# Optimization experiments

Measured on AMD Instinct MI355X. Metric: run time of the kernel, lower is better.

Reference implementation:

```python
import jax, jax.numpy as jnp
import numpy as np

N_HEADS = 16
D_K = 64
D_V = 64
HIDDEN = 1024
B, S = 2, 2048
LN_EPS = 1e-5


def setup_inputs() -> dict:
    key = jax.random.key(0)
    ks = jax.random.split(key, 6)
    inputs = jax.random.normal(ks[0], (B, S, HIDDEN), dtype=jnp.float32)
    attn_mask = jax.random.randint(ks[1], (B, S, S), 0, 2, dtype=jnp.int32)
    scale = 1.0 / np.sqrt(HIDDEN)
    W_Q = jax.random.normal(ks[2], (HIDDEN, HIDDEN), dtype=jnp.float32) * scale
    W_K = jax.random.normal(ks[3], (HIDDEN, HIDDEN), dtype=jnp.float32) * scale
    W_V = jax.random.normal(ks[4], (HIDDEN, HIDDEN), dtype=jnp.float32) * scale
    W_O = jax.random.normal(ks[5], (HIDDEN, HIDDEN), dtype=jnp.float32) * scale
    return {"inputs": inputs, "attn_mask": attn_mask,
            "W_Q": W_Q, "W_K": W_K, "W_V": W_V, "W_O": W_O}


def reference(inputs, attn_mask, W_Q, W_K, W_V, W_O):
    b, s, _ = inputs.shape
    # nn.Linear(bias=False): x @ W.T ; reshape to [B, H, S, d]
    Q = (inputs @ W_Q.T).reshape(b, s, N_HEADS, D_K).transpose(0, 2, 1, 3)
    K = (inputs @ W_K.T).reshape(b, s, N_HEADS, D_K).transpose(0, 2, 1, 3)
    V = (inputs @ W_V.T).reshape(b, s, N_HEADS, D_V).transpose(0, 2, 1, 3)
    scores = jnp.einsum('bhqd,bhkd->bhqk', Q, K) / np.sqrt(D_K)
    mask = (attn_mask == 0)[:, None, :, :]  # broadcast over heads
    scores = jnp.where(mask, jnp.float32(-1e9), scores)
    attn = jax.nn.softmax(scores, axis=-1)
    context = jnp.einsum('bhqk,bhkd->bhqd', attn, V)
    context = context.transpose(0, 2, 1, 3).reshape(b, s, N_HEADS * D_V)
    output = context @ W_O.T
    x = output + inputs  # residual
    # LayerNorm with default weight=1, bias=0, eps=1e-5
    mu = jnp.mean(x, axis=-1, keepdims=True)
    var = jnp.mean(jnp.square(x - mu), axis=-1, keepdims=True)
    out = (x - mu) * jax.lax.rsqrt(var + LN_EPS)
    return out, attn
```

## Files before the change

### kernel.cpp

```cpp
#include <hip/hip_runtime.h>

typedef unsigned short u16;
typedef unsigned long long u64;
typedef __bf16 bf16x8 __attribute__((ext_vector_type(8)));
typedef float f32x4 __attribute__((ext_vector_type(4)));

static __device__ __forceinline__ u16 f32_to_bf16(float f) {
    unsigned u = __builtin_bit_cast(unsigned, f);
    u += 0x7fffu + ((u >> 16) & 1u);
    return (u16)(u >> 16);
}
static __device__ __forceinline__ float bf16_to_f32(u16 v) {
    return __builtin_bit_cast(float, ((unsigned)v) << 16);
}

__global__ __launch_bounds__(256) void cast_f32_bf16(const float* __restrict__ in,
                                                     u16* __restrict__ out, int n)
{
    int i = (blockIdx.x * 256 + threadIdx.x) * 4;
    if (i >= n) return;
    float4 v = *reinterpret_cast<const float4*>(in + i);
    ushort4 o;
    o.x = f32_to_bf16(v.x); o.y = f32_to_bf16(v.y);
    o.z = f32_to_bf16(v.z); o.w = f32_to_bf16(v.w);
    *reinterpret_cast<ushort4*>(out + i) = o;
}

__global__ __launch_bounds__(256) void cast_w4(
    const float* __restrict__ w0, const float* __restrict__ w1,
    const float* __restrict__ w2, const float* __restrict__ w3,
    u16* __restrict__ o0, u16* __restrict__ o1,
    u16* __restrict__ o2, u16* __restrict__ o3)
{
    const float* src; u16* dst;
    switch (blockIdx.y) {
        case 0: src = w0; dst = o0; break;
        case 1: src = w1; dst = o1; break;
        case 2: src = w2; dst = o2; break;
        default: src = w3; dst = o3; break;
    }
    int i = (blockIdx.x * 256 + threadIdx.x) * 4;
    float4 v = *reinterpret_cast<const float4*>(src + i);
    ushort4 o;
    o.x = f32_to_bf16(v.x); o.y = f32_to_bf16(v.y);
    o.z = f32_to_bf16(v.z); o.w = f32_to_bf16(v.w);
    *reinterpret_cast<ushort4*>(dst + i) = o;
}

__global__ __launch_bounds__(256) void pack_mask(const int* __restrict__ mask,
                                                 u64* __restrict__ out)
{
    int t = blockIdx.x * 256 + threadIdx.x;
    const int4* p = reinterpret_cast<const int4*>(mask + (size_t)t * 64);
    u64 bits = 0;
#pragma unroll
    for (int j = 0; j < 16; ++j) {
        int4 v = p[j];
        bits |= ((u64)(v.x != 0)) << (j * 4 + 0);
        bits |= ((u64)(v.y != 0)) << (j * 4 + 1);
        bits |= ((u64)(v.z != 0)) << (j * 4 + 2);
        bits |= ((u64)(v.w != 0)) << (j * 4 + 3);
    }
    out[t] = bits;
}

__global__ __launch_bounds__(256) void gemm128_qkv(
    const u16* __restrict__ A,
    const u16* __restrict__ BQ, const u16* __restrict__ BK, const u16* __restrict__ BV,
    u16* __restrict__ CQ, u16* __restrict__ CK, u16* __restrict__ CV)
{
    constexpr int N = 1024, K = 1024;
    const u16* B; u16* C;
    switch (blockIdx.z) {
        case 0:  B = BQ; C = CQ; break;
        case 1:  B = BK; C = CK; break;
        default: B = BV; C = CV; break;
    }
    __shared__ __align__(16) u16 As[128][64];
    __shared__ __align__(16) u16 Bs[128][64];
    const int tid  = threadIdx.x;
    const int wave = tid >> 6, lane = tid & 63;
    const int quad = lane >> 4, l16 = lane & 15;
    const int wr = wave >> 1, wc = wave & 1;
    const int m0 = blockIdx.y * 128, n0 = blockIdx.x * 128;

    f32x4 acc[4][4] = {};
    const int srow = tid >> 3;
    const int scol = (tid & 7) * 8;
    const u16* Ap = A + (size_t)(m0 + srow) * K + scol;
    const u16* Bp = B + (size_t)(n0 + srow) * K + scol;
    u16* AsW = &As[0][0] + wave * 512;
    u16* BsW = &Bs[0][0] + wave * 512;

    for (int k0 = 0; k0 < K; k0 += 64) {
        __syncthreads();
#pragma unroll
        for (int j = 0; j < 4; ++j) {
            __builtin_amdgcn_global_load_lds(
                (const __attribute__((address_space(1))) unsigned*)(Ap + (size_t)(32 * j) * K + k0),
                (__attribute__((address_space(3))) unsigned*)(AsW + j * 2048),
                16, 0, 0);
            __builtin_amdgcn_global_load_lds(
                (const __attribute__((address_space(1))) unsigned*)(Bp + (size_t)(32 * j) * K + k0),
                (__attribute__((address_space(3))) unsigned*)(BsW + j * 2048),
                16, 0, 0);
        }
        __syncthreads();
#pragma unroll
        for (int ks = 0; ks < 2; ++ks) {
            bf16x8 a[4], bb[4];
#pragma unroll
            for (int mi = 0; mi < 4; ++mi)
                a[mi] = *reinterpret_cast<const bf16x8*>(&As[wr * 64 + mi * 16 + l16][ks * 32 + quad * 8]);
#pragma unroll
            for (int ni = 0; ni < 4; ++ni)
                bb[ni] = *reinterpret_cast<const bf16x8*>(&Bs[wc * 64 + ni * 16 + l16][ks * 32 + quad * 8]);
#pragma unroll
            for (int mi = 0; mi < 4; ++mi)
#pragma unroll
                for (int ni = 0; ni < 4; ++ni)
                    acc[mi][ni] = __builtin_amdgcn_mfma_f32_16x16x32_bf16(a[mi], bb[ni], acc[mi][ni], 0, 0, 0);
        }
    }
#pragma unroll
    for (int mi = 0; mi < 4; ++mi)
#pragma unroll
        for (int ni = 0; ni < 4; ++ni)
#pragma unroll
            for (int r = 0; r < 4; ++r) {
                int row = m0 + wr * 64 + mi * 16 + quad * 4 + r;
                int col = n0 + wc * 64 + ni * 16 + l16;
                C[(size_t)row * N + col] = f32_to_bf16(acc[mi][ni][r]);
            }
}

__global__ __launch_bounds__(256) void gemm128_res(
    const u16* __restrict__ A, const u16* __restrict__ B,
    const float* __restrict__ X, float* __restrict__ C)
{
    constexpr int N = 1024, K = 1024;
    __shared__ __align__(16) u16 As[128][64];
    __shared__ __align__(16) u16 Bs[128][64];
    const int tid  = threadIdx.x;
    const int wave = tid >> 6, lane = tid & 63;
    const int quad = lane >> 4, l16 = lane & 15;
    const int wr = wave >> 1, wc = wave & 1;
    const int m0 = blockIdx.y * 128, n0 = blockIdx.x * 128;

    f32x4 acc[4][4] = {};
    const int srow = tid >> 3;
    const int scol = (tid & 7) * 8;
    const u16* Ap = A + (size_t)(m0 + srow) * K + scol;
    const u16* Bp = B + (size_t)(n0 + srow) * K + scol;
    u16* AsW = &As[0][0] + wave * 512;
    u16* BsW = &Bs[0][0] + wave * 512;

    for (int k0 = 0; k0 < K; k0 += 64) {
        __syncthreads();
#pragma unroll
        for (int j = 0; j < 4; ++j) {
            __builtin_amdgcn_global_load_lds(
                (const __attribute__((address_space(1))) unsigned*)(Ap + (size_t)(32 * j) * K + k0),
                (__attribute__((address_space(3))) unsigned*)(AsW + j * 2048),
                16, 0, 0);
            __builtin_amdgcn_global_load_lds(
                (const __attribute__((address_space(1))) unsigned*)(Bp + (size_t)(32 * j) * K + k0),
                (__attribute__((address_space(3))) unsigned*)(BsW + j * 2048),
                16, 0, 0);
        }
        __syncthreads();
#pragma unroll
        for (int ks = 0; ks < 2; ++ks) {
            bf16x8 a[4], bb[4];
#pragma unroll
            for (int mi = 0; mi < 4; ++mi)
                a[mi] = *reinterpret_cast<const bf16x8*>(&As[wr * 64 + mi * 16 + l16][ks * 32 + quad * 8]);
#pragma unroll
            for (int ni = 0; ni < 4; ++ni)
                bb[ni] = *reinterpret_cast<const bf16x8*>(&Bs[wc * 64 + ni * 16 + l16][ks * 32 + quad * 8]);
#pragma unroll
            for (int mi = 0; mi < 4; ++mi)
#pragma unroll
                for (int ni = 0; ni < 4; ++ni)
                    acc[mi][ni] = __builtin_amdgcn_mfma_f32_16x16x32_bf16(a[mi], bb[ni], acc[mi][ni], 0, 0, 0);
        }
    }
#pragma unroll
    for (int mi = 0; mi < 4; ++mi)
#pragma unroll
        for (int ni = 0; ni < 4; ++ni)
#pragma unroll
            for (int r = 0; r < 4; ++r) {
                int row = m0 + wr * 64 + mi * 16 + quad * 4 + r;
                int col = n0 + wc * 64 + ni * 16 + l16;
                C[(size_t)row * N + col] = acc[mi][ni][r] + X[(size_t)row * N + col];
            }
}

__global__ __launch_bounds__(256) void transpose_v(const u16* __restrict__ Vw,
                                                   u16* __restrict__ VT)
{
    constexpr int S = 2048, HID = 1024, NH = 16;
    __shared__ __align__(16) u16 Ts[64][72];
    const int tid = threadIdx.x;
    const int lr = tid >> 2, lc = (tid & 3) * 16;
    const int st = blockIdx.x, h = blockIdx.y, b = blockIdx.z;
    {
        const u16* p = Vw + ((size_t)(b * S + st * 64 + lr)) * HID + h * 64 + lc;
        *reinterpret_cast<int4*>(&Ts[lr][lc])     = *reinterpret_cast<const int4*>(p);
        *reinterpret_cast<int4*>(&Ts[lr][lc + 8]) = *reinterpret_cast<const int4*>(p + 8);
    }
    __syncthreads();
    u16* q = VT + ((size_t)((b * NH + h) * 64 + lr)) * S + st * 64 + lc;
    union { int4 v; u16 s[8]; } o0, o1;
#pragma unroll
    for (int j = 0; j < 8; ++j) o0.s[j] = Ts[lc + j][lr];
#pragma unroll
    for (int j = 0; j < 8; ++j) o1.s[j] = Ts[lc + 8 + j][lr];
    *reinterpret_cast<int4*>(q)     = o0.v;
    *reinterpret_cast<int4*>(q + 8) = o1.v;
}

__global__ __launch_bounds__(256) void attn_kernel(
    const u16* __restrict__ Q, const u16* __restrict__ K,
    const u16* __restrict__ VT, const u64* __restrict__ Mb,
    float* __restrict__ attn_out, u16* __restrict__ ctx_out)
{
    constexpr int S = 2048, HID = 1024, NH = 16;
    __shared__ __align__(16) u16 Qs[64][72];
    __shared__ __align__(16) u16 Ks[64][72];
    __shared__ __align__(16) u16 Vs[64][72];
    __shared__ __align__(16) u16 Ps[64][72];

    const int tid  = threadIdx.x;
    const int wave = tid >> 6, lane = tid & 63;
    const int quad = lane >> 4, l16 = lane & 15;

    const int flat = (blockIdx.z * NH + blockIdx.y) * (S / 64) + blockIdx.x;
    const int s_id = (flat & 7) * 128 + (flat >> 3);
    const int qt = s_id & 31, h = (s_id >> 5) & 15, b = s_id >> 9;

    const size_t qkv_base = (size_t)b * S * HID + h * 64;
    const size_t vt_base  = ((size_t)(b * NH + h)) * 64 * S;

    const int lr = tid >> 2;
    const int lc = (tid & 3) * 16;
    {
        const u16* p = Q + qkv_base + (size_t)(qt * 64 + lr) * HID + lc;
        *reinterpret_cast<int4*>(&Qs[lr][lc])     = *reinterpret_cast<const int4*>(p);
        *reinterpret_cast<int4*>(&Qs[lr][lc + 8]) = *reinterpret_cast<const int4*>(p + 8);
    }

    const int q_row0 = qt * 64 + wave * 16 + quad * 4;
    const size_t mrow = (size_t)b * S + q_row0;

    const u16* Kp = K + qkv_base + (size_t)lr * HID + lc;
    const u16* Vp = VT + vt_base + (size_t)lr * S + lc;

    float l_acc[4] = {0.f, 0.f, 0.f, 0.f};

    int4 kc0 = *reinterpret_cast<const int4*>(Kp);
    int4 kc1 = *reinterpret_cast<const int4*>(Kp + 8);
    for (int kt = 0; kt < S / 64; ++kt) {
        u64 mw[4];
#pragma unroll
        for (int r = 0; r < 4; ++r) mw[r] = Mb[(mrow + r) * 32 + kt];
        __syncthreads();
        *reinterpret_cast<int4*>(&Ks[lr][lc])     = kc0;
        *reinterpret_cast<int4*>(&Ks[lr][lc + 8]) = kc1;
        int4 kn0, kn1;
        if (kt < S / 64 - 1) {
            const u16* p = Kp + (size_t)(kt + 1) * 64 * HID;
            kn0 = *reinterpret_cast<const int4*>(p);
            kn1 = *reinterpret_cast<const int4*>(p + 8);
        } else { kn0 = kc0; kn1 = kc1; }
        __syncthreads();
        f32x4 sc[4] = {};
#pragma unroll
        for (int ks = 0; ks < 2; ++ks) {
            bf16x8 a = *reinterpret_cast<const bf16x8*>(&Qs[wave * 16 + l16][ks * 32 + quad * 8]);
#pragma unroll
            for (int cb = 0; cb < 4; ++cb) {
                bf16x8 bb = *reinterpret_cast<const bf16x8*>(&Ks[cb * 16 + l16][ks * 32 + quad * 8]);
                sc[cb] = __builtin_amdgcn_mfma_f32_16x16x32_bf16(a, bb, sc[cb], 0, 0, 0);
            }
        }
#pragma unroll
        for (int cb = 0; cb < 4; ++cb) {
            int bi = cb * 16 + l16;
#pragma unroll
            for (int r = 0; r < 4; ++r) {
                float pe = ((mw[r] >> bi) & 1ull)
                               ? __expf(fmaf(sc[cb][r], 0.125f, -16.f)) : 0.f;
                l_acc[r] += pe;
            }
        }
        kc0 = kn0; kc1 = kn1;
    }
    float rl[4];
#pragma unroll
    for (int r = 0; r < 4; ++r) {
        float s = l_acc[r];
        s += __shfl_xor(s, 1);
        s += __shfl_xor(s, 2);
        s += __shfl_xor(s, 4);
        s += __shfl_xor(s, 8);
        rl[r] = 1.0f / s;
    }

    f32x4 ctx[4] = {};
    kc0 = *reinterpret_cast<const int4*>(Kp);
    kc1 = *reinterpret_cast<const int4*>(Kp + 8);
    int4 vc0 = *reinterpret_cast<const int4*>(Vp);
    int4 vc1 = *reinterpret_cast<const int4*>(Vp + 8);
    for (int kt = 0; kt < S / 64; ++kt) {
        u64 mw[4];
#pragma unroll
        for (int r = 0; r < 4; ++r) mw[r] = Mb[(mrow + r) * 32 + kt];
        __syncthreads();
        *reinterpret_cast<int4*>(&Ks[lr][lc])     = kc0;
        *reinterpret_cast<int4*>(&Ks[lr][lc + 8]) = kc1;
        *reinterpret_cast<int4*>(&Vs[lr][lc])     = vc0;
        *reinterpret_cast<int4*>(&Vs[lr][lc + 8]) = vc1;
        int4 kn0, kn1, vn0, vn1;
        if (kt < S / 64 - 1) {
            const u16* p = Kp + (size_t)(kt + 1) * 64 * HID;
            kn0 = *reinterpret_cast<const int4*>(p);
            kn1 = *reinterpret_cast<const int4*>(p + 8);
            const u16* pv = Vp + (kt + 1) * 64;
            vn0 = *reinterpret_cast<const int4*>(pv);
            vn1 = *reinterpret_cast<const int4*>(pv + 8);
        } else { kn0 = kc0; kn1 = kc1; vn0 = vc0; vn1 = vc1; }
        __syncthreads();
        f32x4 sc[4] = {};
#pragma unroll
        for (int ks = 0; ks < 2; ++ks) {
            bf16x8 a = *reinterpret_cast<const bf16x8*>(&Qs[wave * 16 + l16][ks * 32 + quad * 8]);
#pragma unroll
            for (int cb = 0; cb < 4; ++cb) {
                bf16x8 bb = *reinterpret_cast<const bf16x8*>(&Ks[cb * 16 + l16][ks * 32 + quad * 8]);
                sc[cb] = __builtin_amdgcn_mfma_f32_16x16x32_bf16(a, bb, sc[cb], 0, 0, 0);
            }
        }
#pragma unroll
        for (int cb = 0; cb < 4; ++cb) {
            int bi = cb * 16 + l16;
#pragma unroll
            for (int r = 0; r < 4; ++r) {
                float pe = ((mw[r] >> bi) & 1ull)
                               ? __expf(fmaf(sc[cb][r], 0.125f, -16.f)) * rl[r] : 0.f;
                Ps[wave * 16 + quad * 4 + r][cb * 16 + l16] = f32_to_bf16(pe);
            }
        }
        asm volatile("s_waitcnt lgkmcnt(0)" ::: "memory");
        __builtin_amdgcn_sched_barrier(0);
        {
            size_t arow = (((size_t)(b * NH + h) * S) + qt * 64 + lr) * S + kt * 64 + lc;
#pragma unroll
            for (int g = 0; g < 4; ++g) {
                float4 o;
                o.x = bf16_to_f32(Ps[lr][lc + g * 4 + 0]);
                o.y = bf16_to_f32(Ps[lr][lc + g * 4 + 1]);
                o.z = bf16_to_f32(Ps[lr][lc + g * 4 + 2]);
                o.w = bf16_to_f32(Ps[lr][lc + g * 4 + 3]);
                *reinterpret_cast<float4*>(&attn_out[arow + g * 4]) = o;
            }
        }
#pragma unroll
        for (int ks = 0; ks < 2; ++ks) {
            bf16x8 a = *reinterpret_cast<const bf16x8*>(&Ps[wave * 16 + l16][ks * 32 + quad * 8]);
#pragma unroll
            for (int cb = 0; cb < 4; ++cb) {
                bf16x8 bb = *reinterpret_cast<const bf16x8*>(&Vs[cb * 16 + l16][ks * 32 + quad * 8]);
                ctx[cb] = __builtin_amdgcn_mfma_f32_16x16x32_bf16(a, bb, ctx[cb], 0, 0, 0);
            }
        }
        kc0 = kn0; kc1 = kn1; vc0 = vn0; vc1 = vn1;
    }
#pragma unroll
    for (int cb = 0; cb < 4; ++cb)
#pragma unroll
        for (int r = 0; r < 4; ++r) {
            int q = q_row0 + r;
            int d = cb * 16 + l16;
            ctx_out[qkv_base + (size_t)q * HID + d] = f32_to_bf16(ctx[cb][r]);
        }
}

__global__ __launch_bounds__(256) void ln_kernel(const float* __restrict__ X,
                                                 float* __restrict__ out)
{
    __shared__ float red[8];
    const int row = blockIdx.x;
    const int tid = threadIdx.x;
    const int wave = tid >> 6, lane = tid & 63;
    const float* xr = X + (size_t)row * 1024;
    float v[4];
    float s = 0.f;
#pragma unroll
    for (int i = 0; i < 4; ++i) { v[i] = xr[tid + 256 * i]; s += v[i]; }
#pragma unroll
    for (int off = 1; off < 64; off <<= 1) s += __shfl_xor(s, off);
    if (lane == 0) red[wave] = s;
    __syncthreads();
    float mean = (red[0] + red[1] + red[2] + red[3]) * (1.0f / 1024.0f);
    float s2 = 0.f;
#pragma unroll
    for (int i = 0; i < 4; ++i) { float d = v[i] - mean; s2 += d * d; }
#pragma unroll
    for (int off = 1; off < 64; off <<= 1) s2 += __shfl_xor(s2, off);
    if (lane == 0) red[4 + wave] = s2;
    __syncthreads();
    float var = (red[4] + red[5] + red[6] + red[7]) * (1.0f / 1024.0f);
    float rstd = rsqrtf(var + 1e-5f);
#pragma unroll
    for (int i = 0; i < 4; ++i)
        out[(size_t)row * 1024 + tid + 256 * i] = (v[i] - mean) * rstd;
}

extern "C" void kernel_launch(void* const* d_in, const int* in_sizes, int n_in,
                              void* d_out, int out_size, void* d_ws, size_t ws_size,
                              hipStream_t stream)
{
    constexpr int B = 2, S = 2048, HID = 1024, NH = 16;
    constexpr int M = B * S;

    const float* X  = (const float*)d_in[0];
    const int* mask = (const int*)d_in[1];
    const float* WQ = (const float*)d_in[2];
    const float* WK = (const float*)d_in[3];
    const float* WV = (const float*)d_in[4];
    const float* WO = (const float*)d_in[5];

    float* out  = (float*)d_out;
    float* attn = out + (size_t)M * HID;

    u64*   Mb  = (u64*)d_ws;
    u16*   Xb  = (u16*)(Mb + (size_t)B * S * 32);
    u16*   WQb = Xb  + (size_t)M * HID;
    u16*   WKb = WQb + (size_t)HID * HID;
    u16*   WVb = WKb + (size_t)HID * HID;
    u16*   WOb = WVb + (size_t)HID * HID;
    u16*   Qw  = WOb + (size_t)HID * HID;
    u16*   Kw  = Qw  + (size_t)M * HID;
    u16*   Vw  = Kw  + (size_t)M * HID;
    u16*   Cw  = Vw  + (size_t)M * HID;
    u16*   VT  = Xb;
    float* XO  = (float*)Qw;

    dim3 blk(256);
    cast_f32_bf16<<<dim3((M * HID) / 1024), blk, 0, stream>>>(X, Xb, M * HID);
    cast_w4<<<dim3((HID * HID) / 1024, 4), blk, 0, stream>>>(WQ, WK, WV, WO,
                                                             WQb, WKb, WVb, WOb);
    pack_mask<<<dim3((B * S * 32) / 256), blk, 0, stream>>>(mask, Mb);

    gemm128_qkv<<<dim3(HID / 128, M / 128, 3), blk, 0, stream>>>(Xb, WQb, WKb, WVb,
                                                                 Qw, Kw, Vw);
    transpose_v<<<dim3(S / 64, NH, B), blk, 0, stream>>>(Vw, VT);

    attn_kernel<<<dim3(S / 64, NH, B), blk, 0, stream>>>(Qw, Kw, VT, Mb, attn, Cw);

    gemm128_res<<<dim3(HID / 128, M / 128), blk, 0, stream>>>(Cw, WOb, X, XO);
    ln_kernel<<<dim3(M), blk, 0, stream>>>(XO, out);
}
```

Before: 844.7 us.

## Pre-swizzle K and V into MFMA fragment layout, load directly to registers

A prep kernel now rewrites K and V into per-tile MFMA operand order, replacing the old V transpose. The attention kernel then loads K and V fragments straight from global memory into registers and keeps Q fragments in registers. This removes the shared-memory staging and two barriers per tile. The trade-off is that each of the four waves now fetches the full K/V tile separately and the explicit software prefetch is gone, so latency hiding depends on cache hits and occupancy. The extra Vf buffer also enlarges the workspace.

Measured after the change: 880.9 us. 4.3% more time.

```diff
diff --git a/kernel.cpp b/kernel.cpp
--- a/kernel.cpp
+++ b/kernel.cpp
@@ -197,39 +197,47 @@
             }
 }
 
-__global__ __launch_bounds__(256) void transpose_v(const u16* __restrict__ Vw,
-                                                   u16* __restrict__ VT)
+__global__ __launch_bounds__(256) void prep_kv(const u16* __restrict__ Kw,
+                                               const u16* __restrict__ Vw,
+                                               u16* __restrict__ Kf,
+                                               u16* __restrict__ Vf)
 {
     constexpr int S = 2048, HID = 1024, NH = 16;
-    __shared__ __align__(16) u16 Ts[64][72];
+    __shared__ __align__(16) u16 Kt[64][72];
+    __shared__ __align__(16) u16 Vt[64][72];
     const int tid = threadIdx.x;
+    const int kt = blockIdx.x, h = blockIdx.y, b = blockIdx.z;
     const int lr = tid >> 2, lc = (tid & 3) * 16;
-    const int st = blockIdx.x, h = blockIdx.y, b = blockIdx.z;
     {
-        const u16* p = Vw + ((size_t)(b * S + st * 64 + lr)) * HID + h * 64 + lc;
-        *reinterpret_cast<int4*>(&Ts[lr][lc])     = *reinterpret_cast<const int4*>(p);
-        *reinterpret_cast<int4*>(&Ts[lr][lc + 8]) = *reinterpret_cast<const int4*>(p + 8);
+        const u16* pk = Kw + ((size_t)(b * S + kt * 64 + lr)) * HID + h * 64 + lc;
+        *reinterpret_cast<int4*>(&Kt[lr][lc])     = *reinterpret_cast<const int4*>(pk);
+        *reinterpret_cast<int4*>(&Kt[lr][lc + 8]) = *reinterpret_cast<const int4*>(pk + 8);
+        const u16* pv = Vw + ((size_t)(b * S + kt * 64 + lr)) * HID + h * 64 + lc;
+        *reinterpret_cast<int4*>(&Vt[lr][lc])     = *reinterpret_cast<const int4*>(pv);
+        *reinterpret_cast<int4*>(&Vt[lr][lc + 8]) = *reinterpret_cast<const int4*>(pv + 8);
     }
     __syncthreads();
-    u16* q = VT + ((size_t)((b * NH + h) * 64 + lr)) * S + st * 64 + lc;
-    union { int4 v; u16 s[8]; } o0, o1;
-#pragma unroll
-    for (int j = 0; j < 8; ++j) o0.s[j] = Ts[lc + j][lr];
-#pragma unroll
-    for (int j = 0; j < 8; ++j) o1.s[j] = Ts[lc + 8 + j][lr];
-    *reinterpret_cast<int4*>(q)     = o0.v;
-    *reinterpret_cast<int4*>(q + 8) = o1.v;
+    const size_t fbase = (((size_t)(b * NH + h)) * 32 + kt) * 4096;
+    for (int c = tid; c < 512; c += 256) {
+        int frag = c >> 6;
+        int lane = c & 63;
+        int l16 = lane & 15, quad = lane >> 4;
+        int ks = frag >> 2, cb = frag & 3;
+        *reinterpret_cast<int4*>(Kf + fbase + (size_t)c * 8) =
+            *reinterpret_cast<const int4*>(&Kt[cb * 16 + l16][ks * 32 + quad * 8]);
+        u16 tmp[8];
+#pragma unroll
+        for (int e = 0; e < 8; ++e) tmp[e] = Vt[ks * 32 + quad * 8 + e][cb * 16 + l16];
+        *reinterpret_cast<int4*>(Vf + fbase + (size_t)c * 8) = *reinterpret_cast<int4*>(tmp);
+    }
 }
 
 __global__ __launch_bounds__(256) void attn_kernel(
-    const u16* __restrict__ Q, const u16* __restrict__ K,
-    const u16* __restrict__ VT, const u64* __restrict__ Mb,
+    const u16* __restrict__ Qw, const u16* __restrict__ Kf,
+    const u16* __restrict__ Vf, const u64* __restrict__ Mb,
     float* __restrict__ attn_out, u16* __restrict__ ctx_out)
 {
     constexpr int S = 2048, HID = 1024, NH = 16;
-    __shared__ __align__(16) u16 Qs[64][72];
-    __shared__ __align__(16) u16 Ks[64][72];
-    __shared__ __align__(16) u16 Vs[64][72];
     __shared__ __align__(16) u16 Ps[64][72];
 
     const int tid  = threadIdx.x;
@@ -241,50 +249,34 @@
     const int qt = s_id & 31, h = (s_id >> 5) & 15, b = s_id >> 9;
 
     const size_t qkv_base = (size_t)b * S * HID + h * 64;
-    const size_t vt_base  = ((size_t)(b * NH + h)) * 64 * S;
-
-    const int lr = tid >> 2;
-    const int lc = (tid & 3) * 16;
-    {
-        const u16* p = Q + qkv_base + (size_t)(qt * 64 + lr) * HID + lc;
-        *reinterpret_cast<int4*>(&Qs[lr][lc])     = *reinterpret_cast<const int4*>(p);
-        *reinterpret_cast<int4*>(&Qs[lr][lc + 8]) = *reinterpret_cast<const int4*>(p + 8);
-    }
+    const size_t f_base   = ((size_t)(b * NH + h)) * 131072;
+
+    bf16x8 qf[2];
+#pragma unroll
+    for (int ks = 0; ks < 2; ++ks)
+        qf[ks] = *reinterpret_cast<const bf16x8*>(
+            Qw + qkv_base + (size_t)(qt * 64 + wave * 16 + l16) * HID + ks * 32 + quad * 8);
 
     const int q_row0 = qt * 64 + wave * 16 + quad * 4;
     const size_t mrow = (size_t)b * S + q_row0;
 
-    const u16* Kp = K + qkv_base + (size_t)lr * HID + lc;
-    const u16* Vp = VT + vt_base + (size_t)lr * S + lc;
-
     float l_acc[4] = {0.f, 0.f, 0.f, 0.f};
 
-    int4 kc0 = *reinterpret_cast<const int4*>(Kp);
-    int4 kc1 = *reinterpret_cast<const int4*>(Kp + 8);
     for (int kt = 0; kt < S / 64; ++kt) {
+        const u16* kfp = Kf + f_base + (size_t)kt * 4096 + lane * 8;
+        bf16x8 kf[8];
+#pragma unroll
+        for (int f = 0; f < 8; ++f)
+            kf[f] = *reinterpret_cast<const bf16x8*>(kfp + f * 512);
         u64 mw[4];
 #pragma unroll
         for (int r = 0; r < 4; ++r) mw[r] = Mb[(mrow + r) * 32 + kt];
-        __syncthreads();
-        *reinterpret_cast<int4*>(&Ks[lr][lc])     = kc0;
-        *reinterpret_cast<int4*>(&Ks[lr][lc + 8]) = kc1;
-        int4 kn0, kn1;
-        if (kt < S / 64 - 1) {
-            const u16* p = Kp + (size_t)(kt + 1) * 64 * HID;
-            kn0 = *reinterpret_cast<const int4*>(p);
-            kn1 = *reinterpret_cast<const int4*>(p + 8);
-        } else { kn0 = kc0; kn1 = kc1; }
-        __syncthreads();
         f32x4 sc[4] = {};
 #pragma unroll
-        for (int ks = 0; ks < 2; ++ks) {
-            bf16x8 a = *reinterpret_cast<const bf16x8*>(&Qs[wave * 16 + l16][ks * 32 + quad * 8]);
-#pragma unroll
-            for (int cb = 0; cb < 4; ++cb) {
-                bf16x8 bb = *reinterpret_cast<const bf16x8*>(&Ks[cb * 16 + l16][ks * 32 + quad * 8]);
-                sc[cb] = __builtin_amdgcn_mfma_f32_16x16x32_bf16(a, bb, sc[cb], 0, 0, 0);
-            }
-        }
+        for (int ks = 0; ks < 2; ++ks)
+#pragma unroll
+            for (int cb = 0; cb < 4; ++cb)
+                sc[cb] = __builtin_amdgcn_mfma_f32_16x16x32_bf16(qf[ks], kf[ks * 4 + cb], sc[cb], 0, 0, 0);
 #pragma unroll
         for (int cb = 0; cb < 4; ++cb) {
             int bi = cb * 16 + l16;
@@ -295,7 +287,6 @@
                 l_acc[r] += pe;
             }
         }
-        kc0 = kn0; kc1 = kn1;
     }
     float rl[4];
 #pragma unroll
@@ -308,40 +299,27 @@
         rl[r] = 1.0f / s;
     }
 
+    const int lr = tid >> 2;
+    const int lc = (tid & 3) * 16;
     f32x4 ctx[4] = {};
-    kc0 = *reinterpret_cast<const int4*>(Kp);
-    kc1 = *reinterpret_cast<const int4*>(Kp + 8);
-    int4 vc0 = *reinterpret_cast<const int4*>(Vp);
-    int4 vc1 = *reinterpret_cast<const int4*>(Vp + 8);
     for (int kt = 0; kt < S / 64; ++kt) {
+        const u16* kfp = Kf + f_base + (size_t)kt * 4096 + lane * 8;
+        const u16* vfp = Vf + f_base + (size_t)kt * 4096 + lane * 8;
+        bf16x8 kf[8], vf[8];
+#pragma unroll
+        for (int f = 0; f < 8; ++f) {
+            kf[f] = *reinterpret_cast<const bf16x8*>(kfp + f * 512);
+            vf[f] = *reinterpret_cast<const bf16x8*>(vfp + f * 512);
+        }
         u64 mw[4];
 #pragma unroll
         for (int r = 0; r < 4; ++r) mw[r] = Mb[(mrow + r) * 32 + kt];
-        __syncthreads();
-        *reinterpret_cast<int4*>(&Ks[lr][lc])     = kc0;
-        *reinterpret_cast<int4*>(&Ks[lr][lc + 8]) = kc1;
-        *reinterpret_cast<int4*>(&Vs[lr][lc])     = vc0;
-        *reinterpret_cast<int4*>(&Vs[lr][lc + 8]) = vc1;
-        int4 kn0, kn1, vn0, vn1;
-        if (kt < S / 64 - 1) {
-            const u16* p = Kp + (size_t)(kt + 1) * 64 * HID;
-            kn0 = *reinterpret_cast<const int4*>(p);
-            kn1 = *reinterpret_cast<const int4*>(p + 8);
-            const u16* pv = Vp + (kt + 1) * 64;
-            vn0 = *reinterpret_cast<const int4*>(pv);
-            vn1 = *reinterpret_cast<const int4*>(pv + 8);
-        } else { kn0 = kc0; kn1 = kc1; vn0 = vc0; vn1 = vc1; }
-        __syncthreads();
         f32x4 sc[4] = {};
 #pragma unroll
-        for (int ks = 0; ks < 2; ++ks) {
-            bf16x8 a = *reinterpret_cast<const bf16x8*>(&Qs[wave * 16 + l16][ks * 32 + quad * 8]);
-#pragma unroll
-            for (int cb = 0; cb < 4; ++cb) {
-                bf16x8 bb = *reinterpret_cast<const bf16x8*>(&Ks[cb * 16 + l16][ks * 32 + quad * 8]);
-                sc[cb] = __builtin_amdgcn_mfma_f32_16x16x32_bf16(a, bb, sc[cb], 0, 0, 0);
-            }
-        }
+        for (int ks = 0; ks < 2; ++ks)
+#pragma unroll
+            for (int cb = 0; cb < 4; ++cb)
+                sc[cb] = __builtin_amdgcn_mfma_f32_16x16x32_bf16(qf[ks], kf[ks * 4 + cb], sc[cb], 0, 0, 0);
 #pragma unroll
         for (int cb = 0; cb < 4; ++cb) {
             int bi = cb * 16 + l16;
@@ -370,12 +348,9 @@
         for (int ks = 0; ks < 2; ++ks) {
             bf16x8 a = *reinterpret_cast<const bf16x8*>(&Ps[wave * 16 + l16][ks * 32 + quad * 8]);
 #pragma unroll
-            for (int cb = 0; cb < 4; ++cb) {
-                bf16x8 bb = *reinterpret_cast<const bf16x8*>(&Vs[cb * 16 + l16][ks * 32 + quad * 8]);
-                ctx[cb] = __builtin_amdgcn_mfma_f32_16x16x32_bf16(a, bb, ctx[cb], 0, 0, 0);
-            }
-        }
-        kc0 = kn0; kc1 = kn1; vc0 = vn0; vc1 = vn1;
+            for (int cb = 0; cb < 4; ++cb)
+                ctx[cb] = __builtin_amdgcn_mfma_f32_16x16x32_bf16(a, vf[ks * 4 + cb], ctx[cb], 0, 0, 0);
+        }
     }
 #pragma unroll
     for (int cb = 0; cb < 4; ++cb)
@@ -445,7 +420,8 @@
     u16*   Kw  = Qw  + (size_t)M * HID;
     u16*   Vw  = Kw  + (size_t)M * HID;
     u16*   Cw  = Vw  + (size_t)M * HID;
-    u16*   VT  = Xb;
+    u16*   Vf  = Cw  + (size_t)M * HID;
+    u16*   Kf  = Xb;
     float* XO  = (float*)Qw;
 
     dim3 blk(256);
@@ -456,9 +432,9 @@
 
     gemm128_qkv<<<dim3(HID / 128, M / 128, 3), blk, 0, stream>>>(Xb, WQb, WKb, WVb,
                                                                  Qw, Kw, Vw);
-    transpose_v<<<dim3(S / 64, NH, B), blk, 0, stream>>>(Vw, VT);
-
-    attn_kernel<<<dim3(S / 64, NH, B), blk, 0, stream>>>(Qw, Kw, VT, Mb, attn, Cw);
+    prep_kv<<<dim3(S / 64, NH, B), blk, 0, stream>>>(Kw, Vw, Kf, Vf);
+
+    attn_kernel<<<dim3(S / 64, NH, B), blk, 0, stream>>>(Qw, Kf, Vf, Mb, attn, Cw);
 
     gemm128_res<<<dim3(HID / 128, M / 128), blk, 0, stream>>>(Cw, WOb, X, XO);
     ln_kernel<<<dim3(M), blk, 0, stream>>>(XO, out);
```
